# Kernel optimization log

Hardware: AMD Instinct MI355X
Metric: run time of the kernel (lower is better)

Reference implementation:

```python
import jax, jax.numpy as jnp
import numpy as np

NW = 30000   # window nodes
NE = 30000   # example nodes
E  = 480000  # edges per relation (avg degree 16)
H  = 512     # hidden_channels
L  = 4       # num_layers
SLOPE = 0.2
LAM = 0.5    # CSRA residual attention weight


def _segment_mean(x, idx, n):
    s = jax.ops.segment_sum(x, idx, num_segments=n)
    c = jax.ops.segment_sum(jnp.ones((idx.shape[0], 1), x.dtype), idx, num_segments=n)
    return s / jnp.maximum(c, 1.0)


def _sage(x_src, x_dst, edge, Wl, Wr, b, n_dst):
    # PyG SAGEConv: lin_l(mean_agg(x_j)) + lin_r(x_i)
    agg = _segment_mean(x_src[edge[0]], edge[1], n_dst)  # [n_dst, H]
    return agg @ Wl + b + x_dst @ Wr


def setup_inputs() -> dict:
    key = jax.random.key(0)
    ks = jax.random.split(key, 24)
    s = 0.02
    nrm = lambda k, shape: (jax.random.normal(k, shape, jnp.float32) * s)
    return {
        "x_window": jax.random.normal(ks[0], (NW, 1949), jnp.float32),
        "x_example": jax.random.normal(ks[1], (NE, 100), jnp.float32),
        "edge_near": jax.random.randint(ks[2], (2, E), 0, NW, jnp.int32),
        "edge_close": jax.random.randint(ks[3], (2, E), 0, NE, jnp.int32),
        "edge_refer": jax.random.randint(ks[4], (2, E), 0, NW, jnp.int32),  # src=example, dst=window
        "W_win": nrm(ks[5], (1949, H)),
        "W_exp": nrm(ks[6], (100, H)),
        "W_post": nrm(ks[7], (H, H)),
        "W_ey": nrm(ks[8], (250, H)),
        "Wl_near": nrm(ks[9], (L, H, H)),
        "Wr_near": nrm(ks[10], (L, H, H)),
        "b_near": jnp.zeros((L, H), jnp.float32),
        "Wl_close": nrm(ks[11], (L, H, H)),
        "Wr_close": nrm(ks[12], (L, H, H)),
        "b_close": jnp.zeros((L, H), jnp.float32),
        "Wl_refer": nrm(ks[13], (L, H, H)),
        "Wr_refer": nrm(ks[14], (L, H, H)),
        "b_refer": jnp.zeros((L, H), jnp.float32),
        "w_pool": nrm(ks[15], (H,)),
        "W_lin": nrm(ks[16], (H, 100)),
        "b_lin": jnp.zeros((100,), jnp.float32),
    }


def reference(x_window, x_example, edge_near, edge_close, edge_refer,
              W_win, W_exp, W_post, W_ey,
              Wl_near, Wr_near, b_near,
              Wl_close, Wr_close, b_close,
              Wl_refer, Wr_refer, b_refer,
              w_pool, W_lin, b_lin):
    lrelu = lambda x: jax.nn.leaky_relu(x, SLOPE)
    post = lambda h: lrelu(lrelu(h) @ W_post)  # LeakyReLU -> Linear -> LeakyReLU

    h_exp = post(x_example @ W_exp)            # [NE, H]
    h_win = post(x_window @ W_win)             # [NW, H]
    # example_y is computed in the original but dropped by HeteroConv (no conv
    # targets it); compute for faithfulness, unused.
    _example_y = h_exp[:, -250:] @ W_ey

    for l in range(L):
        o_near = _sage(h_win, h_win, edge_near, Wl_near[l], Wr_near[l], b_near[l], NW)
        o_refer = _sage(h_exp, h_win, edge_refer, Wl_refer[l], Wr_refer[l], b_refer[l], NW)
        o_close = _sage(h_exp, h_exp, edge_close, Wl_close[l], Wr_close[l], b_close[l], NE)
        h_win = lrelu((o_near + o_refer) * 0.5)  # HeteroConv aggr='mean' over 2 relations
        h_exp = lrelu(o_close)

    # CSRA-style pooling: residual attention over 'refer' edges into window nodes
    src, dst = edge_refer[0], edge_refer[1]
    score = h_exp @ w_pool                      # [NE]
    s = score[src]                              # [E]
    m = jax.ops.segment_max(s, dst, num_segments=NW)
    ex = jnp.exp(s - m[dst])
    z = jax.ops.segment_sum(ex, dst, num_segments=NW)
    att = ex / jnp.maximum(z[dst], 1e-12)
    pooled = jax.ops.segment_sum(att[:, None] * h_exp[src], dst, num_segments=NW)
    out = h_win + LAM * pooled                  # [NW, H]
    return out @ W_lin + b_lin                  # [NW, 100]
```

## Files before the change

kernel.cpp:

```cpp
#include <hip/hip_runtime.h>
#include <hip/hip_bf16.h>
#include <cstdint>
#include <cstddef>

#define NW 30000
#define NE 30000
#define EE 480000
#define HD 512
#define NL 4
#define SLOPE 0.2f
#define LAM 0.5f
#define ROWP 30080
#define MT 235
#define WHH ((size_t)HD * HD)

typedef short short8 __attribute__((ext_vector_type(8)));
typedef float f32x4 __attribute__((ext_vector_type(4)));

static __device__ __forceinline__ float lrelu_f(float x){
    return fmaxf(x, 0.f) + SLOPE * fminf(x, 0.f);
}
static __device__ __forceinline__ short f2bf(float f){
    uint32_t u = __builtin_bit_cast(uint32_t, f);
    u += 0x7FFFu + ((u >> 16) & 1u);
    return (short)(u >> 16);
}
static __device__ __forceinline__ float bf2f(short s){
    uint32_t u = ((uint32_t)(uint16_t)s) << 16;
    return __builtin_bit_cast(float, u);
}

typedef const __attribute__((address_space(1))) void* gas_t;
typedef __attribute__((address_space(3))) void* las_t;
static __device__ __forceinline__ void gload16(const void* g, void* l){
    __builtin_amdgcn_global_load_lds((gas_t)g, (las_t)l, 16, 0, 0);
}


__global__ void count_kernel(const int* __restrict__ dst, int* __restrict__ deg, int E){
    int e = blockIdx.x * 256 + threadIdx.x;
    if (e < E) atomicAdd(&deg[dst[e]], 1);
}

__global__ void scan3_kernel(const int* d0, int n0, int* o0,
                             const int* d1, int n1, int* o1,
                             const int* d2, int n2, int* o2){
    const int* deg; int n; int* off;
    if (blockIdx.x == 0){ deg=d0; n=n0; off=o0; }
    else if (blockIdx.x == 1){ deg=d1; n=n1; off=o1; }
    else { deg=d2; n=n2; off=o2; }
    __shared__ int tmp[1024];
    int t = threadIdx.x;
    int carry = 0;
    if (t == 0) off[0] = 0;
    for (int base = 0; base < n; base += 1024){
        int v = (base + t < n) ? deg[base + t] : 0;
        tmp[t] = v; __syncthreads();
        for (int d = 1; d < 1024; d <<= 1){
            int add = (t >= d) ? tmp[t - d] : 0;
            __syncthreads();
            tmp[t] += add;
            __syncthreads();
        }
        if (base + t < n) off[base + t + 1] = tmp[t] + carry;
        carry += tmp[1023];
        __syncthreads();
    }
}

__global__ void fill_kernel(const int* __restrict__ src, const int* __restrict__ dst,
                            int* __restrict__ cur, const int* __restrict__ off,
                            int* __restrict__ elist, int E){
    int e = blockIdx.x * 256 + threadIdx.x;
    if (e < E){
        int d = dst[e];
        int p = atomicAdd(&cur[d], 1);
        elist[off[d] + p] = src[e];
    }
}


__global__ __launch_bounds__(256)
void transpose_bf_kernel(const float* __restrict__ in, short* __restrict__ out,
                         int K, int N, int Kpad){
    __shared__ float tile[32][33];
    int kbase = blockIdx.y * 32, nbase = blockIdx.x * 32;
    int tx = threadIdx.x & 31, ty = threadIdx.x >> 5;
    #pragma unroll
    for (int r = 0; r < 4; ++r){
        int k = kbase + ty + r * 8;
        float v = 0.f;
        if (k < K) v = in[(size_t)k * N + nbase + tx];
        tile[ty + r * 8][tx] = v;
    }
    __syncthreads();
    #pragma unroll
    for (int r = 0; r < 4; ++r){
        int n = nbase + ty + r * 8;
        int k = kbase + tx;
        if (k < Kpad) out[(size_t)n * Kpad + k] = f2bf(tile[tx][ty + r * 8]);
    }
}


__global__ __launch_bounds__(256)
void transpose_all_kernel(const float* __restrict__ Wln, const float* __restrict__ Wlr,
                          const float* __restrict__ Wlc, const float* __restrict__ Wrc,
                          const float* __restrict__ Wrn, const float* __restrict__ Wrr,
                          const float* __restrict__ Wpost, short* __restrict__ outT){
    __shared__ float tile[32][33];
    int z = blockIdx.z;
    const float* a; const float* b = nullptr;
    if (z < 4) a = Wln + (size_t)z * WHH;
    else if (z < 8) a = Wlr + (size_t)(z - 4) * WHH;
    else if (z < 12) a = Wlc + (size_t)(z - 8) * WHH;
    else if (z < 16) a = Wrc + (size_t)(z - 12) * WHH;
    else if (z < 20){ a = Wrn + (size_t)(z - 16) * WHH; b = Wrr + (size_t)(z - 16) * WHH; }
    else a = Wpost;
    short* outp = outT + (size_t)z * WHH;
    int kbase = blockIdx.y * 32, nbase = blockIdx.x * 32;
    int tx = threadIdx.x & 31, ty = threadIdx.x >> 5;
    #pragma unroll
    for (int r = 0; r < 4; ++r){
        int k = kbase + ty + r * 8;
        float v = a[(size_t)k * HD + nbase + tx];
        if (b) v += b[(size_t)k * HD + nbase + tx];
        tile[ty + r * 8][tx] = v;
    }
    __syncthreads();
    #pragma unroll
    for (int r = 0; r < 4; ++r){
        int n = nbase + ty + r * 8;
        outp[(size_t)n * HD + kbase + tx] = f2bf(tile[tx][ty + r * 8]);
    }
}

__global__ void addf_kernel(const float* __restrict__ a, const float* __restrict__ b,
                            float* __restrict__ o, int n){
    int i = blockIdx.x * 256 + threadIdx.x;
    if (i < n) o[i] = a[i] + b[i];
}


__global__ __launch_bounds__(256)
void conv_xw_kernel(const float* __restrict__ x, short* __restrict__ o){
    int idx = blockIdx.x * 256 + threadIdx.x;
    if (idx >= 30000 * 244) return;
    int row = idx / 244, c8 = idx - row * 244;
    int base = c8 * 8;
    short8 v = {};
    const float* xp = x + (size_t)row * 1949 + base;
    if (base + 8 <= 1949){
        f32x4 a = *(const f32x4*)xp;
        f32x4 bq = *(const f32x4*)(xp + 4);
        #pragma unroll
        for (int j = 0; j < 4; ++j){ v[j] = f2bf(a[j]); v[j + 4] = f2bf(bq[j]); }
    } else {
        #pragma unroll
        for (int j = 0; j < 8; ++j) if (base + j < 1949) v[j] = f2bf(xp[j]);
    }
    *(short8*)(o + (size_t)row * 1952 + base) = v;
}


__global__ __launch_bounds__(256)
void conv_xe_kernel(const float* __restrict__ x, short* __restrict__ o){
    int idx = blockIdx.x * 256 + threadIdx.x;
    if (idx >= ROWP * 16) return;
    int row = idx >> 4, c8 = idx & 15;
    int base = c8 * 8;
    short8 v = {};
    if (row < 30000){
        const float* xp = x + (size_t)row * 100 + base;
        #pragma unroll
        for (int j = 0; j < 8; ++j) if (base + j < 100) v[j] = f2bf(xp[j]);
    }
    *(short8*)(o + (size_t)row * 128 + base) = v;
}


__global__ __launch_bounds__(256)
void seg_mean3_kernel(const short* __restrict__ hw, const short* __restrict__ he,
                      const int* __restrict__ off_n, const int* __restrict__ el_n,
                      const int* __restrict__ off_r, const int* __restrict__ el_r,
                      const int* __restrict__ off_c, const int* __restrict__ el_c,
                      short* __restrict__ aggA, short* __restrict__ aggB, short* __restrict__ aggC){
    int slot = blockIdx.x * 4 + (threadIdx.x >> 6);
    int lane = threadIdx.x & 63;
    if (slot >= 3 * NW) return;
    int seg = slot / NW;
    int dst = slot - seg * NW;
    const short* h; const int* off; const int* el; short* out;
    if (seg == 0){ h = hw; off = off_n; el = el_n; out = aggA; }
    else if (seg == 1){ h = he; off = off_r; el = el_r; out = aggB; }
    else { h = he; off = off_c; el = el_c; out = aggC; }
    int s0 = off[dst], s1 = off[dst + 1];
    float acc[8] = {};
    int e = s0;
    for (; e + 8 <= s1; e += 8){
        int idx[8];
        #pragma unroll
        for (int u = 0; u < 8; ++u) idx[u] = el[e + u];
        short8 v[8];
        #pragma unroll
        for (int u = 0; u < 8; ++u) v[u] = *(const short8*)(h + (size_t)idx[u] * HD + lane * 8);
        #pragma unroll
        for (int u = 0; u < 8; ++u)
            #pragma unroll
            for (int j = 0; j < 8; ++j) acc[j] += bf2f(v[u][j]);
    }
    for (; e < s1; ++e){
        short8 v = *(const short8*)(h + (size_t)el[e] * HD + lane * 8);
        #pragma unroll
        for (int j = 0; j < 8; ++j) acc[j] += bf2f(v[j]);
    }
    float inv = (s1 > s0) ? 1.0f / (float)(s1 - s0) : 0.0f;
    short8 o8;
    #pragma unroll
    for (int j = 0; j < 8; ++j) o8[j] = f2bf(acc[j] * inv);
    *(short8*)(out + (size_t)dst * HD + lane * 8) = o8;
}


template<int DUAL>
__global__ __launch_bounds__(256)
void mgemm2_kernel(
    const short* __restrict__ a00, const short* __restrict__ a01, const short* __restrict__ a02,
    const short* __restrict__ b00, const short* __restrict__ b01, const short* __restrict__ b02,
    const float* __restrict__ bias0, short* __restrict__ c160, float* __restrict__ c320,
    int np0, int kt0, int act0,
    const short* __restrict__ a10, const short* __restrict__ a11, const short* __restrict__ a12,
    const short* __restrict__ b10, const short* __restrict__ b11, const short* __restrict__ b12,
    const float* __restrict__ bias1, short* __restrict__ c161, float* __restrict__ c321,
    int np1, int kt1, int act1,
    int mreal){
    __shared__ short lds[16384];
    short* ldsA = lds;
    short* ldsB = lds + 8192;

    int nwg = gridDim.x, orig = blockIdx.x;
    int q = nwg >> 3, r = nwg & 7;
    int xcd = orig & 7, lid = orig >> 3;
    int logical = (xcd < r ? xcd * (q + 1) : r * (q + 1) + (xcd - r) * q) + lid;
    int mtile = logical >> 2, nc = logical & 3;
    int dsel, ml;
    if (DUAL){ dsel = mtile & 1; ml = mtile >> 1; } else { dsel = 0; ml = mtile; }

    const short* A0 = dsel ? a10 : a00;
    const short* A1 = dsel ? a11 : a01;
    const short* A2 = dsel ? a12 : a02;
    const short* B0 = dsel ? b10 : b00;
    const short* B1 = dsel ? b11 : b01;
    const short* B2 = dsel ? b12 : b02;
    const float* bias = dsel ? bias1 : bias0;
    short* C16 = dsel ? c161 : c160;
    float* C32 = dsel ? c321 : c320;
    const int np = dsel ? np1 : np0;
    const int kt = dsel ? kt1 : kt0;
    const int act = dsel ? act1 : act0;

    const int row0 = ml * 128, n0 = nc * 128;
    const int t = threadIdx.x, wid = t >> 6, lane = t & 63;
    const int wm = (wid >> 1) * 64, wn = (wid & 1) * 64;
    const int lg = lane >> 4, lr = lane & 15;
    f32x4 acc[4][4] = {};

    int rowi[2], ci[2];
    #pragma unroll
    for (int i = 0; i < 2; ++i){
        int sl = i * 256 + t;
        rowi[i] = sl >> 2;
        ci[i] = (sl & 3) ^ ((rowi[i] >> 1) & 3);
    }
    const int kpt = kt >> 5;
    const int nsteps = np * kpt;

    const short* Acur = A0;
    const short* Bcur = B0;
    int sk = 0, sp = 0, sbuf = 0;

    auto stage = [&](){
        int k0 = sk * 32;
        #pragma unroll
        for (int i = 0; i < 2; ++i){
            int ao = (row0 + rowi[i]) * kt + k0 + ci[i] * 8;
            gload16(Acur + ao, &ldsA[sbuf * 4096 + (i * 256 + wid * 64) * 8]);
        }
        #pragma unroll
        for (int i = 0; i < 2; ++i){
            int bo = (n0 + rowi[i]) * kt + k0 + ci[i] * 8;
            gload16(Bcur + bo, &ldsB[sbuf * 4096 + (i * 256 + wid * 64) * 8]);
        }
        sbuf ^= 1;
        if (++sk == kpt){
            sk = 0; ++sp;
            Acur = (sp == 1) ? A1 : A2;
            Bcur = (sp == 1) ? B1 : B2;
        }
    };
    auto compute = [&](int bb){
        const char* baseA = (const char*)&ldsA[bb * 4096];
        const char* baseB = (const char*)&ldsB[bb * 4096];
        short8 af[4], bfr[4];
        #pragma unroll
        for (int f = 0; f < 4; ++f){
            int rowA = wm + f * 16 + lr;
            af[f] = *(const short8*)(baseA + rowA * 64 + ((lg ^ ((rowA >> 1) & 3)) << 4));
            int rowB = wn + f * 16 + lr;
            bfr[f] = *(const short8*)(baseB + rowB * 64 + ((lg ^ ((rowB >> 1) & 3)) << 4));
        }
        #pragma unroll
        for (int i = 0; i < 4; ++i)
            #pragma unroll
            for (int j = 0; j < 4; ++j)
                acc[i][j] = __builtin_amdgcn_mfma_f32_16x16x32_bf16(af[i], bfr[j], acc[i][j], 0, 0, 0);
    };

    stage();
    for (int s = 0; s < nsteps; ++s){
        if (s + 1 < nsteps){
            stage();
            asm volatile("s_waitcnt vmcnt(4)" ::: "memory");
        } else {
            asm volatile("s_waitcnt vmcnt(0)" ::: "memory");
        }
        __builtin_amdgcn_s_barrier();
        __builtin_amdgcn_sched_barrier(0);
        compute(s & 1);
        asm volatile("s_waitcnt lgkmcnt(0)" ::: "memory");
        __builtin_amdgcn_sched_barrier(0);
        __builtin_amdgcn_s_barrier();
    }

    float bv[4];
    #pragma unroll
    for (int f = 0; f < 4; ++f) bv[f] = bias ? bias[n0 + wn + f * 16 + lr] : 0.f;
    #pragma unroll
    for (int i = 0; i < 4; ++i){
        #pragma unroll
        for (int r2 = 0; r2 < 4; ++r2){
            int gr = row0 + wm + i * 16 + lg * 4 + r2;
            #pragma unroll
            for (int j = 0; j < 4; ++j){
                int gc = n0 + wn + j * 16 + lr;
                float v = acc[i][j][r2] + bv[j];
                if (act == 2) v *= 0.5f;
                if (act) v = lrelu_f(v);
                C16[(size_t)gr * HD + gc] = f2bf(v);
                if (C32 && gr < mreal) C32[(size_t)gr * HD + gc] = v;
            }
        }
    }
}


__global__ __launch_bounds__(128)
void mgemm_af32_kernel(const float* __restrict__ A0, const short* __restrict__ B0,
                       short* __restrict__ C16, int M){
    constexpr int KT = 1952, KACT = 1949, KPT = KT / 32, NSTEPS = KPT, N = 512;
    __shared__ short ldsA[2][2048];
    __shared__ short ldsB[2][4096];
    int nwg = gridDim.x;
    int orig = blockIdx.x;
    int q = nwg >> 3, r = nwg & 7;
    int xcd = orig & 7, lid = orig >> 3;
    int logical = (xcd < r ? xcd * (q + 1) : r * (q + 1) + (xcd - r) * q) + lid;
    const int m0 = (logical >> 2) * 64, n0 = (logical & 3) * 128;
    const int t = threadIdx.x, wid = t >> 6, lane = t & 63;
    const int wn = wid * 64;
    const int lg = lane >> 4, lr = lane & 15;
    f32x4 acc[4][4] = {};
    int rowiA[2], ciA[2];
    #pragma unroll
    for (int i = 0; i < 2; ++i){
        int sl = i * 128 + t;
        rowiA[i] = sl >> 2;
        ciA[i] = (sl & 3) ^ ((rowiA[i] >> 1) & 3);
    }
    int rowiB[4], ciB[4];
    #pragma unroll
    for (int i = 0; i < 4; ++i){
        int sl = i * 128 + t;
        rowiB[i] = sl >> 2;
        ciB[i] = (sl & 3) ^ ((rowiB[i] >> 1) & 3);
    }
    f32x4 ra[2][2];
    auto stage_load = [&](int s){
        int k0 = s * 32;
        int bb = s & 1;
        #pragma unroll
        for (int i = 0; i < 2; ++i){
            int gr = m0 + rowiA[i];
            int gk = k0 + ciA[i] * 8;
            ra[i][0] = (f32x4){0,0,0,0};
            ra[i][1] = (f32x4){0,0,0,0};
            if (gr < M){
                const float* ap = A0 + (size_t)gr * KACT + gk;
                if (gk + 8 <= KACT){
                    ra[i][0] = *(const f32x4*)ap;
                    ra[i][1] = *(const f32x4*)(ap + 4);
                } else {
                    #pragma unroll
                    for (int j = 0; j < 8; ++j)
                        if (gk + j < KACT) ra[i][j >> 2][j & 3] = ap[j];
                }
            }
        }
        #pragma unroll
        for (int i = 0; i < 4; ++i)
            gload16(B0 + (size_t)(n0 + rowiB[i]) * KT + k0 + ciB[i] * 8,
                    &ldsB[bb][(i * 128 + wid * 64) * 8]);
    };
    auto stage_writeA = [&](int s){
        int bb = s & 1;
        #pragma unroll
        for (int i = 0; i < 2; ++i){
            short8 v;
            #pragma unroll
            for (int j = 0; j < 8; ++j) v[j] = f2bf(ra[i][j >> 2][j & 3]);
            *(short8*)&ldsA[bb][(i * 128 + t) * 8] = v;
        }
    };
    auto compute = [&](int s){
        int bb = s & 1;
        short8 af[4], bfr[4];
        #pragma unroll
        for (int f = 0; f < 4; ++f){
            int rowA = f * 16 + lr;
            af[f] = *(const short8*)((const char*)&ldsA[bb][0] + rowA * 64 + ((lg ^ ((rowA >> 1) & 3)) << 4));
            int rowB = wn + f * 16 + lr;
            bfr[f] = *(const short8*)((const char*)&ldsB[bb][0] + rowB * 64 + ((lg ^ ((rowB >> 1) & 3)) << 4));
        }
        #pragma unroll
        for (int i = 0; i < 4; ++i)
            #pragma unroll
            for (int j = 0; j < 4; ++j)
                acc[i][j] = __builtin_amdgcn_mfma_f32_16x16x32_bf16(af[i], bfr[j], acc[i][j], 0, 0, 0);
    };
    stage_load(0);
    stage_writeA(0);
    __syncthreads();
    for (int s = 0; s < NSTEPS; ++s){
        if (s + 1 < NSTEPS) stage_load(s + 1);
        compute(s);
        if (s + 1 < NSTEPS) stage_writeA(s + 1);
        __syncthreads();
    }
    #pragma unroll
    for (int i = 0; i < 4; ++i){
        #pragma unroll
        for (int r2 = 0; r2 < 4; ++r2){
            int gr = m0 + i * 16 + lg * 4 + r2;
            if (gr >= M) continue;
            #pragma unroll
            for (int j = 0; j < 4; ++j){
                int gc = n0 + wn + j * 16 + lr;
                C16[(size_t)gr * N + gc] = f2bf(lrelu_f(acc[i][j][r2]));
            }
        }
    }
}


__global__ __launch_bounds__(256)
void gemm_kernel(const float* __restrict__ A, const float* __restrict__ B,
                 const float* __restrict__ bias, float* __restrict__ C,
                 int M, int N, int K){
    const int BM = 128, BN = 64, BK = 16;
    __shared__ float As[BK][BM];
    __shared__ float Bs[BK][BN];
    int m0 = blockIdx.y * BM, n0 = blockIdx.x * BN;
    int t = threadIdx.x;
    int tx = t & 15, ty = t >> 4;
    float acc[8][4] = {};
    for (int k0 = 0; k0 < K; k0 += BK){
        #pragma unroll
        for (int i = 0; i < 2; ++i){
            int idx = i * 256 + t;
            int row = idx >> 2, kg = idx & 3;
            float4 v = make_float4(0,0,0,0);
            int gr = m0 + row, gk = k0 + kg * 4;
            if (gr < M && gk + 4 <= K)
                v = *reinterpret_cast<const float4*>(A + (size_t)gr * K + gk);
            As[kg*4+0][row] = v.x; As[kg*4+1][row] = v.y;
            As[kg*4+2][row] = v.z; As[kg*4+3][row] = v.w;
        }
        {
            int row = t >> 4, cg = t & 15;
            int gk = k0 + row, col = n0 + cg * 4;
            float4 v = make_float4(0,0,0,0);
            if (gk < K){
                if (col + 4 <= N){
                    v = *reinterpret_cast<const float4*>(B + (size_t)gk * N + col);
                } else {
                    float tp[4] = {0,0,0,0};
                    #pragma unroll
                    for (int j = 0; j < 4; ++j) if (col + j < N) tp[j] = B[(size_t)gk * N + col + j];
                    v = make_float4(tp[0], tp[1], tp[2], tp[3]);
                }
            }
            *reinterpret_cast<float4*>(&Bs[row][cg*4]) = v;
        }
        __syncthreads();
        #pragma unroll
        for (int k = 0; k < BK; ++k){
            float a[8], b[4];
            #pragma unroll
            for (int r = 0; r < 8; ++r) a[r] = As[k][ty*8 + r];
            #pragma unroll
            for (int c = 0; c < 4; ++c) b[c] = Bs[k][tx*4 + c];
            #pragma unroll
            for (int r = 0; r < 8; ++r)
                #pragma unroll
                for (int c = 0; c < 4; ++c)
                    acc[r][c] = fmaf(a[r], b[c], acc[r][c]);
        }
        __syncthreads();
    }
    #pragma unroll
    for (int r = 0; r < 8; ++r){
        int gr = m0 + ty*8 + r;
        if (gr >= M) continue;
        #pragma unroll
        for (int c = 0; c < 4; ++c){
            int gc = n0 + tx*4 + c;
            if (gc >= N) continue;
            C[(size_t)gr * N + gc] = acc[r][c] + bias[gc];
        }
    }
}


template<int F32>
__global__ void score_kernel(const void* __restrict__ hep, const float* __restrict__ w,
                             float* __restrict__ score){
    int row = blockIdx.x * 4 + (threadIdx.x >> 6);
    int lane = threadIdx.x & 63;
    if (row >= NE) return;
    float s = 0.f;
    #pragma unroll
    for (int j = 0; j < 8; ++j){
        int idx = lane + j * 64;
        float x = F32 ? ((const float*)hep)[(size_t)row * HD + idx]
                      : bf2f(((const short*)hep)[(size_t)row * HD + idx]);
        s += x * w[idx];
    }
    #pragma unroll
    for (int off = 32; off > 0; off >>= 1) s += __shfl_down(s, off);
    if (lane == 0) score[row] = s;
}

template<int F32>
__global__ __launch_bounds__(256)
void pool_kernel(const void* __restrict__ hep, const void* __restrict__ hwp,
                 const float* __restrict__ score, const int* __restrict__ off,
                 const int* __restrict__ elist, float* __restrict__ outp){
    int dst = blockIdx.x * 4 + (threadIdx.x >> 6);
    int lane = threadIdx.x & 63;
    if (dst >= NW) return;
    int s0 = off[dst], s1 = off[dst + 1];
    float m = -INFINITY;
    for (int e = s0 + lane; e < s1; e += 64) m = fmaxf(m, score[elist[e]]);
    #pragma unroll
    for (int o = 1; o < 64; o <<= 1) m = fmaxf(m, __shfl_xor(m, o));
    float z = 0.f;
    for (int e = s0 + lane; e < s1; e += 64) z += expf(score[elist[e]] - m);
    #pragma unroll
    for (int o = 1; o < 64; o <<= 1) z += __shfl_xor(z, o);
    float zinv = 1.0f / fmaxf(z, 1e-12f);

    float acc[8] = {};
    int e = s0;
    for (; e + 4 <= s1; e += 4){
        int idx[4]; float at[4];
        #pragma unroll
        for (int u = 0; u < 4; ++u) idx[u] = elist[e + u];
        #pragma unroll
        for (int u = 0; u < 4; ++u) at[u] = expf(score[idx[u]] - m) * zinv;
        #pragma unroll
        for (int u = 0; u < 4; ++u){
            if (F32){
                f32x4 v0 = *(const f32x4*)((const float*)hep + (size_t)idx[u] * HD + lane * 8);
                f32x4 v1 = *(const f32x4*)((const float*)hep + (size_t)idx[u] * HD + lane * 8 + 4);
                #pragma unroll
                for (int k = 0; k < 4; ++k){ acc[k] += at[u] * v0[k]; acc[k+4] += at[u] * v1[k]; }
            } else {
                short8 v = *(const short8*)((const short*)hep + (size_t)idx[u] * HD + lane * 8);
                #pragma unroll
                for (int k = 0; k < 8; ++k) acc[k] += at[u] * bf2f(v[k]);
            }
        }
    }
    for (; e < s1; ++e){
        int src = elist[e];
        float at = expf(score[src] - m) * zinv;
        if (F32){
            f32x4 v0 = *(const f32x4*)((const float*)hep + (size_t)src * HD + lane * 8);
            f32x4 v1 = *(const f32x4*)((const float*)hep + (size_t)src * HD + lane * 8 + 4);
            #pragma unroll
            for (int k = 0; k < 4; ++k){ acc[k] += at * v0[k]; acc[k+4] += at * v1[k]; }
        } else {
            short8 v = *(const short8*)((const short*)hep + (size_t)src * HD + lane * 8);
            #pragma unroll
            for (int k = 0; k < 8; ++k) acc[k] += at * bf2f(v[k]);
        }
    }
    float hw[8];
    if (F32){
        f32x4 v0 = *(const f32x4*)((const float*)hwp + (size_t)dst * HD + lane * 8);
        f32x4 v1 = *(const f32x4*)((const float*)hwp + (size_t)dst * HD + lane * 8 + 4);
        #pragma unroll
        for (int k = 0; k < 4; ++k){ hw[k] = v0[k]; hw[k+4] = v1[k]; }
    } else {
        short8 v = *(const short8*)((const short*)hwp + (size_t)dst * HD + lane * 8);
        #pragma unroll
        for (int k = 0; k < 8; ++k) hw[k] = bf2f(v[k]);
    }
    f32x4 o0, o1;
    #pragma unroll
    for (int k = 0; k < 4; ++k){ o0[k] = hw[k] + LAM * acc[k]; o1[k] = hw[k+4] + LAM * acc[k+4]; }
    *(f32x4*)(outp + (size_t)dst * HD + lane * 8) = o0;
    *(f32x4*)(outp + (size_t)dst * HD + lane * 8 + 4) = o1;
}


extern "C" void kernel_launch(void* const* d_in, const int* in_sizes, int n_in,
                              void* d_out, int out_size, void* d_ws, size_t ws_size,
                              hipStream_t stream){
    const float* x_window = (const float*)d_in[0];
    const float* x_example= (const float*)d_in[1];
    const int*   e_near   = (const int*)d_in[2];
    const int*   e_close  = (const int*)d_in[3];
    const int*   e_refer  = (const int*)d_in[4];
    const float* W_win    = (const float*)d_in[5];
    const float* W_exp    = (const float*)d_in[6];
    const float* W_post   = (const float*)d_in[7];
    const float* Wl_near  = (const float*)d_in[9];
    const float* Wr_near  = (const float*)d_in[10];
    const float* b_near   = (const float*)d_in[11];
    const float* Wl_close = (const float*)d_in[12];
    const float* Wr_close = (const float*)d_in[13];
    const float* b_close  = (const float*)d_in[14];
    const float* Wl_refer = (const float*)d_in[15];
    const float* Wr_refer = (const float*)d_in[16];
    const float* b_refer  = (const float*)d_in[17];
    const float* w_pool   = (const float*)d_in[18];
    const float* W_lin    = (const float*)d_in[19];
    const float* b_lin    = (const float*)d_in[20];
    float* out = (float*)d_out;
    (void)in_sizes; (void)n_in; (void)out_size;

    char* w = (char*)d_ws;
    size_t o = 0;
    auto alloc = [&](size_t bytes)->char*{
        char* p = w + o;
        o += (bytes + 255) & ~(size_t)255;
        return p;
    };
    const size_t HBH = (size_t)ROWP * HD * 2;

    short* h16[2][2];
    h16[0][0] = (short*)alloc(HBH); h16[0][1] = (short*)alloc(HBH);
    h16[1][0] = (short*)alloc(HBH); h16[1][1] = (short*)alloc(HBH);
    short* aggA = (short*)alloc(HBH);
    short* aggB = (short*)alloc(HBH);
    short* aggC = (short*)alloc(HBH);
    float* hwf  = (float*)alloc((size_t)NW * HD * 4);
    short* xe16   = (short*)alloc((size_t)ROWP * 128 * 2);
    short* WwinT  = (short*)alloc((size_t)HD * 1952 * 2);
    short* WexpT  = (short*)alloc((size_t)HD * 128 * 2);
    short* WT     = (short*)alloc((size_t)21 * WHH * 2);
    short* WlnT = WT;
    short* WlrT = WT + 4 * WHH;
    short* WlcT = WT + 8 * WHH;
    short* WrcT = WT + 12 * WHH;
    short* WcbT = WT + 16 * WHH;
    short* WpostT = WT + 20 * WHH;
    float* bsum   = (float*)alloc((size_t)NL * HD * 4);
    float* score  = (float*)alloc((size_t)NE * 4);
    int* degcur = (int*)alloc((size_t)6 * 30000 * 4);
    int* deg_n = degcur, *deg_r = degcur + 30000, *deg_c = degcur + 60000;
    int* cur_n = degcur + 90000, *cur_r = degcur + 120000, *cur_c = degcur + 150000;
    int* off_n = (int*)alloc((size_t)(NW + 1) * 4);
    int* off_r = (int*)alloc((size_t)(NW + 1) * 4);
    int* off_c = (int*)alloc((size_t)(NE + 1) * 4);
    int* el_n  = (int*)alloc((size_t)EE * 4);
    int* el_r  = (int*)alloc((size_t)EE * 4);
    int* el_c  = (int*)alloc((size_t)EE * 4);

    const size_t XWB = (size_t)ROWP * 1952 * 2;
    const size_t HEB = (size_t)NE * HD * 4;
    bool haveXW16 = false, haveF32 = false;
    short* xw16 = nullptr; float* hef = nullptr;
    size_t rem = (ws_size > o) ? ws_size - o : 0;
    if (rem >= XWB + 256){
        char* p = alloc(XWB);
        xw16 = (short*)p; hef = (float*)p;
        haveXW16 = haveF32 = true;
    } else if (rem >= HEB + 256){
        hef = (float*)alloc(HEB);
        haveF32 = true;
    }

    const int* src_n = e_near;  const int* dst_n = e_near + EE;
    const int* src_c = e_close; const int* dst_c = e_close + EE;
    const int* src_r = e_refer; const int* dst_r = e_refer + EE;

    hipMemsetAsync(degcur, 0, (size_t)6 * 30000 * 4, stream);
    int eg = (EE + 255) / 256;
    hipLaunchKernelGGL(count_kernel, dim3(eg), dim3(256), 0, stream, dst_n, deg_n, EE);
    hipLaunchKernelGGL(count_kernel, dim3(eg), dim3(256), 0, stream, dst_r, deg_r, EE);
    hipLaunchKernelGGL(count_kernel, dim3(eg), dim3(256), 0, stream, dst_c, deg_c, EE);
    hipLaunchKernelGGL(scan3_kernel, dim3(3), dim3(1024), 0, stream,
                       deg_n, NW, off_n, deg_r, NW, off_r, deg_c, NE, off_c);
    hipLaunchKernelGGL(fill_kernel, dim3(eg), dim3(256), 0, stream, src_n, dst_n, cur_n, off_n, el_n, EE);
    hipLaunchKernelGGL(fill_kernel, dim3(eg), dim3(256), 0, stream, src_r, dst_r, cur_r, off_r, el_r, EE);
    hipLaunchKernelGGL(fill_kernel, dim3(eg), dim3(256), 0, stream, src_c, dst_c, cur_c, off_c, el_c, EE);

    hipLaunchKernelGGL(transpose_bf_kernel, dim3(16, 61, 1), dim3(256), 0, stream,
                       W_win, WwinT, 1949, HD, 1952);
    hipLaunchKernelGGL(transpose_bf_kernel, dim3(16, 4, 1), dim3(256), 0, stream,
                       W_exp, WexpT, 100, HD, 128);
    hipLaunchKernelGGL(transpose_all_kernel, dim3(16, 16, 21), dim3(256), 0, stream,
                       Wl_near, Wl_refer, Wl_close, Wr_close, Wr_near, Wr_refer, W_post, WT);
    hipLaunchKernelGGL(addf_kernel, dim3((NL * HD + 255) / 256), dim3(256), 0, stream,
                       b_near, b_refer, bsum, NL * HD);
    hipLaunchKernelGGL(conv_xe_kernel, dim3((ROWP * 16 + 255) / 256), dim3(256), 0, stream,
                       x_example, xe16);
    if (haveXW16)
        hipLaunchKernelGGL(conv_xw_kernel, dim3((30000 * 244 + 255) / 256), dim3(256), 0, stream,
                           x_window, xw16);

    const short* z16 = xe16;
    const float* zf = nullptr;

    hipLaunchKernelGGL((mgemm2_kernel<0>), dim3(MT * 4), dim3(256), 0, stream,
        xe16, z16, z16, WexpT, z16, z16, zf, aggA, (float*)nullptr, 1, 128, 1,
        z16, z16, z16, z16, z16, z16, zf, (short*)nullptr, (float*)nullptr, 0, 32, 0, 30000);
    if (haveXW16){
        hipLaunchKernelGGL((mgemm2_kernel<0>), dim3(MT * 4), dim3(256), 0, stream,
            xw16, z16, z16, WwinT, z16, z16, zf, aggB, (float*)nullptr, 1, 1952, 1,
            z16, z16, z16, z16, z16, z16, zf, (short*)nullptr, (float*)nullptr, 0, 32, 0, 30000);
    } else {
        hipLaunchKernelGGL(mgemm_af32_kernel, dim3(4 * ((NW + 63) / 64)), dim3(128), 0, stream,
                           x_window, WwinT, aggB, NW);
    }
    hipLaunchKernelGGL((mgemm2_kernel<1>), dim3(2 * MT * 4), dim3(256), 0, stream,
        aggA, z16, z16, WpostT, z16, z16, zf, h16[1][0], (float*)nullptr, 1, 512, 1,
        aggB, z16, z16, WpostT, z16, z16, zf, h16[0][0], (float*)nullptr, 1, 512, 1, 30000);

    for (int l = 0; l < NL; ++l){
        int cur = l & 1, nxt = cur ^ 1;
        const short* wl_n = WlnT + (size_t)l * WHH;
        const short* wl_r = WlrT + (size_t)l * WHH;
        const short* wl_c = WlcT + (size_t)l * WHH;
        const short* wr_c = WrcT + (size_t)l * WHH;
        const short* wcb  = WcbT + (size_t)l * WHH;
        const float* bs   = bsum + (size_t)l * HD;
        const float* bc   = b_close + (size_t)l * HD;
        bool last = (l == NL - 1);

        hipLaunchKernelGGL(seg_mean3_kernel, dim3((3 * NW + 3) / 4), dim3(256), 0, stream,
                           h16[0][cur], h16[1][cur], off_n, el_n, off_r, el_r, off_c, el_c,
                           aggA, aggB, aggC);
        hipLaunchKernelGGL((mgemm2_kernel<1>), dim3(2 * MT * 4), dim3(256), 0, stream,
            aggA, aggB, h16[0][cur], wl_n, wl_r, wcb, bs, h16[0][nxt],
            last ? hwf : (float*)nullptr, 3, 512, 2,
            aggC, h16[1][cur], z16, wl_c, wr_c, z16, bc, h16[1][nxt],
            (last && haveF32) ? hef : (float*)nullptr, 2, 512, 1, 30000);
    }
    int fin = NL & 1;

    if (haveF32){
        hipLaunchKernelGGL((score_kernel<1>), dim3((NE + 3) / 4), dim3(256), 0, stream,
                           (const void*)hef, w_pool, score);
        hipLaunchKernelGGL((pool_kernel<1>), dim3((NW + 3) / 4), dim3(256), 0, stream,
                           (const void*)hef, (const void*)hwf, score, off_r, el_r, hwf);
    } else {
        hipLaunchKernelGGL((score_kernel<0>), dim3((NE + 3) / 4), dim3(256), 0, stream,
                           (const void*)h16[1][fin], w_pool, score);
        hipLaunchKernelGGL((pool_kernel<0>), dim3((NW + 3) / 4), dim3(256), 0, stream,
                           (const void*)h16[1][fin], (const void*)hwf, score, off_r, el_r, hwf);
    }

    hipLaunchKernelGGL(gemm_kernel, dim3(2, (NW + 127) / 128), dim3(256), 0, stream,
                       hwf, W_lin, b_lin, out, NW, 100, HD);
}
```

Before: 1.861 ms.

## Triple-buffer GEMM LDS stages, merge CSR build kernels, drop fp32 exemplar path

The main GEMM moves from a double-buffered to a triple-buffered LDS ring, which removes the trailing wait and second barrier in each k-step. The per-relation count and fill kernels are merged into single 3-D launches over packed degree, offset and edge-list buffers. The optional fp32 copy of the final example features is dropped, so scoring and pooling always read the bf16 features, and pooling writes to a separate buffer instead of in place. The larger LDS footprint may lower occupancy, and skipping the second barrier is only safe if the three-buffer rotation really keeps loads from overwriting data still being read.

```diff
diff --git a/kernel.cpp b/kernel.cpp
--- a/kernel.cpp
+++ b/kernel.cpp
@@ -37,24 +37,24 @@
 }
 
 
-__global__ void count_kernel(const int* __restrict__ dst, int* __restrict__ deg, int E){
+__global__ void count3_kernel(const int* __restrict__ dn, const int* __restrict__ dr,
+                              const int* __restrict__ dc, int* __restrict__ deg){
+    int z = blockIdx.y;
+    const int* dst = (z == 0) ? dn : ((z == 1) ? dr : dc);
     int e = blockIdx.x * 256 + threadIdx.x;
-    if (e < E) atomicAdd(&deg[dst[e]], 1);
-}
-
-__global__ void scan3_kernel(const int* d0, int n0, int* o0,
-                             const int* d1, int n1, int* o1,
-                             const int* d2, int n2, int* o2){
-    const int* deg; int n; int* off;
-    if (blockIdx.x == 0){ deg=d0; n=n0; off=o0; }
-    else if (blockIdx.x == 1){ deg=d1; n=n1; off=o1; }
-    else { deg=d2; n=n2; off=o2; }
+    if (e < EE) atomicAdd(&deg[z * 30000 + dst[e]], 1);
+}
+
+__global__ void scan3_kernel(const int* __restrict__ deg, int* __restrict__ off3){
+    const int* dg = deg + blockIdx.x * 30000;
+    int* off = off3 + blockIdx.x * (NW + 1);
+    int n = 30000;
     __shared__ int tmp[1024];
     int t = threadIdx.x;
     int carry = 0;
     if (t == 0) off[0] = 0;
     for (int base = 0; base < n; base += 1024){
-        int v = (base + t < n) ? deg[base + t] : 0;
+        int v = (base + t < n) ? dg[base + t] : 0;
         tmp[t] = v; __syncthreads();
         for (int d = 1; d < 1024; d <<= 1){
             int add = (t >= d) ? tmp[t - d] : 0;
@@ -68,14 +68,21 @@
     }
 }
 
-__global__ void fill_kernel(const int* __restrict__ src, const int* __restrict__ dst,
-                            int* __restrict__ cur, const int* __restrict__ off,
-                            int* __restrict__ elist, int E){
+__global__ void fill3_kernel(const int* __restrict__ sn, const int* __restrict__ dn,
+                             const int* __restrict__ sr, const int* __restrict__ dr,
+                             const int* __restrict__ sc, const int* __restrict__ dc,
+                             int* __restrict__ cur, const int* __restrict__ off3,
+                             int* __restrict__ el3){
+    int z = blockIdx.y;
+    const int* src = (z == 0) ? sn : ((z == 1) ? sr : sc);
+    const int* dst = (z == 0) ? dn : ((z == 1) ? dr : dc);
+    const int* off = off3 + z * (NW + 1);
+    int* el = el3 + (size_t)z * EE;
     int e = blockIdx.x * 256 + threadIdx.x;
-    if (e < E){
+    if (e < EE){
         int d = dst[e];
-        int p = atomicAdd(&cur[d], 1);
-        elist[off[d] + p] = src[e];
+        int p = atomicAdd(&cur[z * 30000 + d], 1);
+        el[off[d] + p] = src[e];
     }
 }
 
@@ -181,19 +188,17 @@
 
 __global__ __launch_bounds__(256)
 void seg_mean3_kernel(const short* __restrict__ hw, const short* __restrict__ he,
-                      const int* __restrict__ off_n, const int* __restrict__ el_n,
-                      const int* __restrict__ off_r, const int* __restrict__ el_r,
-                      const int* __restrict__ off_c, const int* __restrict__ el_c,
+                      const int* __restrict__ off3, const int* __restrict__ el3,
                       short* __restrict__ aggA, short* __restrict__ aggB, short* __restrict__ aggC){
     int slot = blockIdx.x * 4 + (threadIdx.x >> 6);
     int lane = threadIdx.x & 63;
     if (slot >= 3 * NW) return;
     int seg = slot / NW;
     int dst = slot - seg * NW;
-    const short* h; const int* off; const int* el; short* out;
-    if (seg == 0){ h = hw; off = off_n; el = el_n; out = aggA; }
-    else if (seg == 1){ h = he; off = off_r; el = el_r; out = aggB; }
-    else { h = he; off = off_c; el = el_c; out = aggC; }
+    const short* h = (seg == 0) ? hw : he;
+    const int* off = off3 + seg * (NW + 1);
+    const int* el = el3 + (size_t)seg * EE;
+    short* out = (seg == 0) ? aggA : ((seg == 1) ? aggB : aggC);
     int s0 = off[dst], s1 = off[dst + 1];
     float acc[8] = {};
     int e = s0;
@@ -234,9 +239,7 @@
     const float* __restrict__ bias1, short* __restrict__ c161, float* __restrict__ c321,
     int np1, int kt1, int act1,
     int mreal){
-    __shared__ short lds[16384];
-    short* ldsA = lds;
-    short* ldsB = lds + 8192;
+    __shared__ short lds[24576];
 
     int nwg = gridDim.x, orig = blockIdx.x;
     int q = nwg >> 3, r = nwg & 7;
@@ -284,23 +287,23 @@
         #pragma unroll
         for (int i = 0; i < 2; ++i){
             int ao = (row0 + rowi[i]) * kt + k0 + ci[i] * 8;
-            gload16(Acur + ao, &ldsA[sbuf * 4096 + (i * 256 + wid * 64) * 8]);
+            gload16(Acur + ao, &lds[sbuf * 4096 + (i * 256 + wid * 64) * 8]);
         }
         #pragma unroll
         for (int i = 0; i < 2; ++i){
             int bo = (n0 + rowi[i]) * kt + k0 + ci[i] * 8;
-            gload16(Bcur + bo, &ldsB[sbuf * 4096 + (i * 256 + wid * 64) * 8]);
-        }
-        sbuf ^= 1;
+            gload16(Bcur + bo, &lds[12288 + sbuf * 4096 + (i * 256 + wid * 64) * 8]);
+        }
+        sbuf = (sbuf == 2) ? 0 : sbuf + 1;
         if (++sk == kpt){
             sk = 0; ++sp;
             Acur = (sp == 1) ? A1 : A2;
             Bcur = (sp == 1) ? B1 : B2;
         }
     };
-    auto compute = [&](int bb){
-        const char* baseA = (const char*)&ldsA[bb * 4096];
-        const char* baseB = (const char*)&ldsB[bb * 4096];
+    auto compute = [&](int cb){
+        const char* baseA = (const char*)(lds + cb * 4096);
+        const char* baseB = (const char*)(lds + 12288 + cb * 4096);
         short8 af[4], bfr[4];
         #pragma unroll
         for (int f = 0; f < 4; ++f){
@@ -317,6 +320,7 @@
     };
 
     stage();
+    int cbuf = 0;
     for (int s = 0; s < nsteps; ++s){
         if (s + 1 < nsteps){
             stage();
@@ -326,10 +330,8 @@
         }
         __builtin_amdgcn_s_barrier();
         __builtin_amdgcn_sched_barrier(0);
-        compute(s & 1);
-        asm volatile("s_waitcnt lgkmcnt(0)" ::: "memory");
-        __builtin_amdgcn_sched_barrier(0);
-        __builtin_amdgcn_s_barrier();
+        compute(cbuf);
+        cbuf = (cbuf == 2) ? 0 : cbuf + 1;
     }
 
     float bv[4];
@@ -531,8 +533,7 @@
 }
 
 
-template<int F32>
-__global__ void score_kernel(const void* __restrict__ hep, const float* __restrict__ w,
+__global__ void score_kernel(const short* __restrict__ he, const float* __restrict__ w,
                              float* __restrict__ score){
     int row = blockIdx.x * 4 + (threadIdx.x >> 6);
     int lane = threadIdx.x & 63;
@@ -541,18 +542,15 @@
     #pragma unroll
     for (int j = 0; j < 8; ++j){
         int idx = lane + j * 64;
-        float x = F32 ? ((const float*)hep)[(size_t)row * HD + idx]
-                      : bf2f(((const short*)hep)[(size_t)row * HD + idx]);
-        s += x * w[idx];
+        s += bf2f(he[(size_t)row * HD + idx]) * w[idx];
     }
     #pragma unroll
     for (int off = 32; off > 0; off >>= 1) s += __shfl_down(s, off);
     if (lane == 0) score[row] = s;
 }
 
-template<int F32>
 __global__ __launch_bounds__(256)
-void pool_kernel(const void* __restrict__ hep, const void* __restrict__ hwp,
+void pool_kernel(const short* __restrict__ he, const float* __restrict__ hwf,
                  const float* __restrict__ score, const int* __restrict__ off,
                  const int* __restrict__ elist, float* __restrict__ outp){
     int dst = blockIdx.x * 4 + (threadIdx.x >> 6);
@@ -579,46 +577,23 @@
         for (int u = 0; u < 4; ++u) at[u] = expf(score[idx[u]] - m) * zinv;
         #pragma unroll
         for (int u = 0; u < 4; ++u){
-            if (F32){
-                f32x4 v0 = *(const f32x4*)((const float*)hep + (size_t)idx[u] * HD + lane * 8);
-                f32x4 v1 = *(const f32x4*)((const float*)hep + (size_t)idx[u] * HD + lane * 8 + 4);
-                #pragma unroll
-                for (int k = 0; k < 4; ++k){ acc[k] += at[u] * v0[k]; acc[k+4] += at[u] * v1[k]; }
-            } else {
-                short8 v = *(const short8*)((const short*)hep + (size_t)idx[u] * HD + lane * 8);
-                #pragma unroll
-                for (int k = 0; k < 8; ++k) acc[k] += at[u] * bf2f(v[k]);
-            }
+            short8 v = *(const short8*)(he + (size_t)idx[u] * HD + lane * 8);
+            #pragma unroll
+            for (int k = 0; k < 8; ++k) acc[k] += at[u] * bf2f(v[k]);
         }
     }
     for (; e < s1; ++e){
         int src = elist[e];
         float at = expf(score[src] - m) * zinv;
-        if (F32){
-            f32x4 v0 = *(const f32x4*)((const float*)hep + (size_t)src * HD + lane * 8);
-            f32x4 v1 = *(const f32x4*)((const float*)hep + (size_t)src * HD + lane * 8 + 4);
-            #pragma unroll
-            for (int k = 0; k < 4; ++k){ acc[k] += at * v0[k]; acc[k+4] += at * v1[k]; }
-        } else {
-            short8 v = *(const short8*)((const short*)hep + (size_t)src * HD + lane * 8);
-            #pragma unroll
-            for (int k = 0; k < 8; ++k) acc[k] += at * bf2f(v[k]);
-        }
-    }
-    float hw[8];
-    if (F32){
-        f32x4 v0 = *(const f32x4*)((const float*)hwp + (size_t)dst * HD + lane * 8);
-        f32x4 v1 = *(const f32x4*)((const float*)hwp + (size_t)dst * HD + lane * 8 + 4);
-        #pragma unroll
-        for (int k = 0; k < 4; ++k){ hw[k] = v0[k]; hw[k+4] = v1[k]; }
-    } else {
-        short8 v = *(const short8*)((const short*)hwp + (size_t)dst * HD + lane * 8);
-        #pragma unroll
-        for (int k = 0; k < 8; ++k) hw[k] = bf2f(v[k]);
-    }
+        short8 v = *(const short8*)(he + (size_t)src * HD + lane * 8);
+        #pragma unroll
+        for (int k = 0; k < 8; ++k) acc[k] += at * bf2f(v[k]);
+    }
+    f32x4 h0 = *(const f32x4*)(hwf + (size_t)dst * HD + lane * 8);
+    f32x4 h1 = *(const f32x4*)(hwf + (size_t)dst * HD + lane * 8 + 4);
     f32x4 o0, o1;
     #pragma unroll
-    for (int k = 0; k < 4; ++k){ o0[k] = hw[k] + LAM * acc[k]; o1[k] = hw[k+4] + LAM * acc[k+4]; }
+    for (int k = 0; k < 4; ++k){ o0[k] = h0[k] + LAM * acc[k]; o1[k] = h1[k] + LAM * acc[k+4]; }
     *(f32x4*)(outp + (size_t)dst * HD + lane * 8) = o0;
     *(f32x4*)(outp + (size_t)dst * HD + lane * 8 + 4) = o1;
 }
@@ -666,6 +641,7 @@
     short* aggB = (short*)alloc(HBH);
     short* aggC = (short*)alloc(HBH);
     float* hwf  = (float*)alloc((size_t)NW * HD * 4);
+    float* pooled = (float*)alloc((size_t)NW * HD * 4);
     short* xe16   = (short*)alloc((size_t)ROWP * 128 * 2);
     short* WwinT  = (short*)alloc((size_t)HD * 1952 * 2);
     short* WexpT  = (short*)alloc((size_t)HD * 128 * 2);
@@ -679,27 +655,19 @@
     float* bsum   = (float*)alloc((size_t)NL * HD * 4);
     float* score  = (float*)alloc((size_t)NE * 4);
     int* degcur = (int*)alloc((size_t)6 * 30000 * 4);
-    int* deg_n = degcur, *deg_r = degcur + 30000, *deg_c = degcur + 60000;
-    int* cur_n = degcur + 90000, *cur_r = degcur + 120000, *cur_c = degcur + 150000;
-    int* off_n = (int*)alloc((size_t)(NW + 1) * 4);
-    int* off_r = (int*)alloc((size_t)(NW + 1) * 4);
-    int* off_c = (int*)alloc((size_t)(NE + 1) * 4);
-    int* el_n  = (int*)alloc((size_t)EE * 4);
-    int* el_r  = (int*)alloc((size_t)EE * 4);
-    int* el_c  = (int*)alloc((size_t)EE * 4);
+    int* deg3 = degcur;
+    int* cur3 = degcur + 90000;
+    int* off3 = (int*)alloc((size_t)3 * (NW + 1) * 4);
+    int* el3  = (int*)alloc((size_t)3 * EE * 4);
+    int* off_r = off3 + (NW + 1);
 
     const size_t XWB = (size_t)ROWP * 1952 * 2;
-    const size_t HEB = (size_t)NE * HD * 4;
-    bool haveXW16 = false, haveF32 = false;
-    short* xw16 = nullptr; float* hef = nullptr;
+    bool haveXW16 = false;
+    short* xw16 = nullptr;
     size_t rem = (ws_size > o) ? ws_size - o : 0;
     if (rem >= XWB + 256){
-        char* p = alloc(XWB);
-        xw16 = (short*)p; hef = (float*)p;
-        haveXW16 = haveF32 = true;
-    } else if (rem >= HEB + 256){
-        hef = (float*)alloc(HEB);
-        haveF32 = true;
+        xw16 = (short*)alloc(XWB);
+        haveXW16 = true;
     }
 
     const int* src_n = e_near;  const int* dst_n = e_near + EE;
@@ -708,14 +676,10 @@
 
     hipMemsetAsync(degcur, 0, (size_t)6 * 30000 * 4, stream);
     int eg = (EE + 255) / 256;
-    hipLaunchKernelGGL(count_kernel, dim3(eg), dim3(256), 0, stream, dst_n, deg_n, EE);
-    hipLaunchKernelGGL(count_kernel, dim3(eg), dim3(256), 0, stream, dst_r, deg_r, EE);
-    hipLaunchKernelGGL(count_kernel, dim3(eg), dim3(256), 0, stream, dst_c, deg_c, EE);
-    hipLaunchKernelGGL(scan3_kernel, dim3(3), dim3(1024), 0, stream,
-                       deg_n, NW, off_n, deg_r, NW, off_r, deg_c, NE, off_c);
-    hipLaunchKernelGGL(fill_kernel, dim3(eg), dim3(256), 0, stream, src_n, dst_n, cur_n, off_n, el_n, EE);
-    hipLaunchKernelGGL(fill_kernel, dim3(eg), dim3(256), 0, stream, src_r, dst_r, cur_r, off_r, el_r, EE);
-    hipLaunchKernelGGL(fill_kernel, dim3(eg), dim3(256), 0, stream, src_c, dst_c, cur_c, off_c, el_c, EE);
+    hipLaunchKernelGGL(count3_kernel, dim3(eg, 3), dim3(256), 0, stream, dst_n, dst_r, dst_c, deg3);
+    hipLaunchKernelGGL(scan3_kernel, dim3(3), dim3(1024), 0, stream, deg3, off3);
+    hipLaunchKernelGGL(fill3_kernel, dim3(eg, 3), dim3(256), 0, stream,
+                       src_n, dst_n, src_r, dst_r, src_c, dst_c, cur3, off3, el3);
 
     hipLaunchKernelGGL(transpose_bf_kernel, dim3(16, 61, 1), dim3(256), 0, stream,
                        W_win, WwinT, 1949, HD, 1952);
@@ -761,28 +725,20 @@
         bool last = (l == NL - 1);
 
         hipLaunchKernelGGL(seg_mean3_kernel, dim3((3 * NW + 3) / 4), dim3(256), 0, stream,
-                           h16[0][cur], h16[1][cur], off_n, el_n, off_r, el_r, off_c, el_c,
-                           aggA, aggB, aggC);
+                           h16[0][cur], h16[1][cur], off3, el3, aggA, aggB, aggC);
         hipLaunchKernelGGL((mgemm2_kernel<1>), dim3(2 * MT * 4), dim3(256), 0, stream,
             aggA, aggB, h16[0][cur], wl_n, wl_r, wcb, bs, h16[0][nxt],
             last ? hwf : (float*)nullptr, 3, 512, 2,
             aggC, h16[1][cur], z16, wl_c, wr_c, z16, bc, h16[1][nxt],
-            (last && haveF32) ? hef : (float*)nullptr, 2, 512, 1, 30000);
+            (float*)nullptr, 2, 512, 1, 30000);
     }
     int fin = NL & 1;
 
-    if (haveF32){
-        hipLaunchKernelGGL((score_kernel<1>), dim3((NE + 3) / 4), dim3(256), 0, stream,
-                           (const void*)hef, w_pool, score);
-        hipLaunchKernelGGL((pool_kernel<1>), dim3((NW + 3) / 4), dim3(256), 0, stream,
-                           (const void*)hef, (const void*)hwf, score, off_r, el_r, hwf);
-    } else {
-        hipLaunchKernelGGL((score_kernel<0>), dim3((NE + 3) / 4), dim3(256), 0, stream,
-                           (const void*)h16[1][fin], w_pool, score);
-        hipLaunchKernelGGL((pool_kernel<0>), dim3((NW + 3) / 4), dim3(256), 0, stream,
-                           (const void*)h16[1][fin], (const void*)hwf, score, off_r, el_r, hwf);
-    }
+    hipLaunchKernelGGL(score_kernel, dim3((NE + 3) / 4), dim3(256), 0, stream,
+                       h16[1][fin], w_pool, score);
+    hipLaunchKernelGGL(pool_kernel, dim3((NW + 3) / 4), dim3(256), 0, stream,
+                       h16[1][fin], hwf, score, off_r, el3 + (size_t)EE, pooled);
 
     hipLaunchKernelGGL(gemm_kernel, dim3(2, (NW + 127) / 128), dim3(256), 0, stream,
-                       hwf, W_lin, b_lin, out, NW, 100, HD);
-}
+                       pooled, W_lin, b_lin, out, NW, 100, HD);
+}
```

Measured after the change: 1.763 ms, median of 2. -5.2%, faster.
